# Performance work log

Hardware: AMD Instinct MI355X
Metric: run time of the kernel (lower is better)

The kernel has to match this reference:

```python
import jax, jax.numpy as jnp
import numpy as np

KERNEL_SIZE = 7      # odd, per assert in __init__
MAX_VAL = 1e4        # kornia morphology default max_val


def setup_inputs() -> dict:
    key = jax.random.key(0)
    kx, ka, kb, kc = jax.random.split(key, 4)
    x = jax.random.normal(kx, (8, 64, 256, 256), dtype=jnp.float32)
    k1 = jax.random.uniform(ka, (1,), dtype=jnp.float32)
    k2 = jax.random.uniform(kb, (1,), dtype=jnp.float32)
    k3 = jax.random.uniform(kc, (1,), dtype=jnp.float32)
    return {"x": x, "k1": k1, "k2": k2, "k3": k3}


def _structuring_element(k1, k2, k3):
    k = KERNEL_SIZE
    # torch.arange(-k//2 + 1, k//2 + 1) with floor-div == -(k//2)..k//2 for odd k
    c = jnp.arange(-(k // 2), k // 2 + 1, dtype=jnp.float32)
    xg, yg = jnp.meshgrid(c, c, indexing='xy')
    se = k1[0] * xg ** 2 + 2.0 * k2[0] * xg * yg + k3[0] * yg ** 2
    se = se / se.max()
    return -se  # (k, k)


def reference(x, k1, k2, k3):
    k = KERNEL_SIZE
    se = _structuring_element(k1, k2, k3)
    # flat kernel of ones with center zeroed -> center tap masked to -max_val
    mask = np.ones((k, k), dtype=bool)
    mask[k // 2, k // 2] = False
    neighborhood = jnp.where(jnp.asarray(mask), se, -MAX_VAL)
    nb = neighborhood[::-1, ::-1]  # kornia dilation flips the neighborhood

    pad = k // 2
    # geodesic border for dilation: pad with -max_val
    xp = jnp.pad(x, ((0, 0), (0, 0), (pad, pad), (pad, pad)),
                 constant_values=-MAX_VAL)
    H, W = x.shape[-2], x.shape[-1]
    # fused running max over the k*k taps; avoids materializing the unfold
    out = jnp.full_like(x, -jnp.inf)
    for i in range(k):
        for j in range(k):
            out = jnp.maximum(out, xp[..., i:i + H, j:j + W] + nb[i, j])
    return out
```

## Files before the change

kernel.cpp:

```cpp
#include <hip/hip_runtime.h>


#define MAXV 10000.0f

constexpr int H = 256;
constexpr int W = 256;
constexpr int TILE_ROWS = 16;
constexpr int LDS_ROWS = TILE_ROWS + 6;
constexpr int LDS_STRIDE = 264;
constexpr int ROW_TILES = H / TILE_ROWS;
constexpr int R = 4;

__device__ __forceinline__ float rfl(float x) {
  return __int_as_float(__builtin_amdgcn_readfirstlane(__float_as_int(x)));
}

__global__ __launch_bounds__(256, 6) void morpho_kernel(
    const float* __restrict__ x,
    const float* __restrict__ k1p,
    const float* __restrict__ k2p,
    const float* __restrict__ k3p,
    float* __restrict__ out) {
  __shared__ __align__(16) float tile[LDS_ROWS * LDS_STRIDE];

  const int tid = threadIdx.x;
  const int p = blockIdx.x >> 4;
  const int ty0 = (blockIdx.x & 15) * TILE_ROWS;

  const float* __restrict__ xp = x + (size_t)p * (H * W);
  float* __restrict__ op = out + (size_t)p * (H * W);

  if (tid < LDS_ROWS * 8) {
    const int h = tid & 7;
    const int col = (h < 4) ? h : (256 + h);
    const int r = tid >> 3;
    tile[r * LDS_STRIDE + col] = -MAXV;
  }

  for (int i = tid; i < LDS_ROWS * 64; i += 256) {
    const int r = i >> 6;
    const int c4 = i & 63;
    const int gy = ty0 - 3 + r;
    float4 v;
    if ((unsigned)gy < (unsigned)H) {
      v = *reinterpret_cast<const float4*>(&xp[gy * W + c4 * 4]);
    } else {
      v.x = v.y = v.z = v.w = -MAXV;
    }
    *reinterpret_cast<float4*>(&tile[r * LDS_STRIDE + 4 + c4 * 4]) = v;
  }

  const float k1v = k1p[0], k2v = k2p[0], k3v = k3p[0];
  float se[49];
#pragma unroll
  for (int i = 0; i < 49; ++i) {
    const float xg = (float)(i % 7 - 3);
    const float yg = (float)(i / 7 - 3);
    se[i] = k1v * (xg * xg) + 2.0f * k2v * (xg * yg) + k3v * (yg * yg);
  }
  float m = se[0];
#pragma unroll
  for (int i = 1; i < 49; ++i) m = fmaxf(m, se[i]);
  const float inv = 1.0f / m;
  float w[49];
#pragma unroll
  for (int i = 0; i < 49; ++i) w[i] = rfl((i == 24) ? -MAXV : (0.0f - se[i] * inv));

  __syncthreads();

  const int tx = tid & 63;
  const int g = tid >> 6;
  const int r0 = g * R;

  float acc[R][4];
#pragma unroll
  for (int t = 0; t < R; ++t)
#pragma unroll
    for (int c = 0; c < 4; ++c) acc[t][c] = -INFINITY;

#pragma unroll
  for (int iy = 0; iy < R + 6; ++iy) {
    const float* rp = &tile[(r0 + iy) * LDS_STRIDE + tx * 4];
    float buf[12];
#pragma unroll
    for (int q = 0; q < 3; ++q) {
      const float4 v = *reinterpret_cast<const float4*>(rp + 4 * q);
      buf[4 * q + 0] = v.x;
      buf[4 * q + 1] = v.y;
      buf[4 * q + 2] = v.z;
      buf[4 * q + 3] = v.w;
    }
#pragma unroll
    for (int t = 0; t < R; ++t) {
      const int dyr = iy - t;
      if (dyr < 0 || dyr > 6) continue;
#pragma unroll
      for (int c = 0; c < 4; ++c) {
        const float s0 = buf[c + 1] + w[dyr * 7 + 0];
        const float s1 = buf[c + 2] + w[dyr * 7 + 1];
        const float s2 = buf[c + 3] + w[dyr * 7 + 2];
        const float s3 = buf[c + 4] + w[dyr * 7 + 3];
        const float s4 = buf[c + 5] + w[dyr * 7 + 4];
        const float s5 = buf[c + 6] + w[dyr * 7 + 5];
        const float s6 = buf[c + 7] + w[dyr * 7 + 6];
        const float m0 = fmaxf(fmaxf(s0, s1), s2);
        const float m1 = fmaxf(fmaxf(s3, s4), s5);
        const float m01 = fmaxf(m0, m1);
        acc[t][c] = fmaxf(acc[t][c], fmaxf(m01, s6));
      }
    }
  }

#pragma unroll
  for (int t = 0; t < R; ++t) {
    const int gy = ty0 + r0 + t;
    float4 v;
    v.x = acc[t][0];
    v.y = acc[t][1];
    v.z = acc[t][2];
    v.w = acc[t][3];
    *reinterpret_cast<float4*>(&op[gy * W + tx * 4]) = v;
  }
}

extern "C" void kernel_launch(void* const* d_in, const int* in_sizes, int n_in,
                              void* d_out, int out_size, void* d_ws, size_t ws_size,
                              hipStream_t stream) {
  const float* x = (const float*)d_in[0];
  const float* k1 = (const float*)d_in[1];
  const float* k2 = (const float*)d_in[2];
  const float* k3 = (const float*)d_in[3];
  float* outp = (float*)d_out;

  const int planes = 8 * 64;
  const int blocks = planes * ROW_TILES;
  morpho_kernel<<<dim3(blocks), dim3(256), 0, stream>>>(x, k1, k2, k3, outp);
}
```

Baseline: 287.1 us.

## Load tile via direct global-to-LDS loads, lane-parallel weights, nontemporal stores

```diff
diff --git a/kernel.cpp b/kernel.cpp
--- a/kernel.cpp
+++ b/kernel.cpp
@@ -11,8 +11,12 @@
 constexpr int ROW_TILES = H / TILE_ROWS;
 constexpr int R = 4;
 
-__device__ __forceinline__ float rfl(float x) {
-  return __int_as_float(__builtin_amdgcn_readfirstlane(__float_as_int(x)));
+typedef float vfloat4 __attribute__((ext_vector_type(4)));
+
+__device__ __forceinline__ void load_lds16(const float* g, float* l) {
+  __builtin_amdgcn_global_load_lds(
+      (const __attribute__((address_space(1))) void*)g,
+      (__attribute__((address_space(3))) void*)l, 16, 0, 0);
 }
 
 __global__ __launch_bounds__(256, 6) void morpho_kernel(
@@ -24,53 +28,52 @@
   __shared__ __align__(16) float tile[LDS_ROWS * LDS_STRIDE];
 
   const int tid = threadIdx.x;
+  const int lane = tid & 63;
+  const int wid = tid >> 6;
   const int p = blockIdx.x >> 4;
   const int ty0 = (blockIdx.x & 15) * TILE_ROWS;
 
   const float* __restrict__ xp = x + (size_t)p * (H * W);
   float* __restrict__ op = out + (size_t)p * (H * W);
 
+  for (int r = wid; r < LDS_ROWS; r += 4) {
+    const int gy = ty0 - 3 + r;
+    float* ldst = &tile[r * LDS_STRIDE + 4];
+    if ((unsigned)gy < (unsigned)H) {
+      load_lds16(&xp[gy * W + lane * 4], ldst);
+    } else {
+      vfloat4 mv = {-MAXV, -MAXV, -MAXV, -MAXV};
+      *reinterpret_cast<vfloat4*>(ldst + lane * 4) = mv;
+    }
+  }
+
   if (tid < LDS_ROWS * 8) {
     const int h = tid & 7;
     const int col = (h < 4) ? h : (256 + h);
-    const int r = tid >> 3;
-    tile[r * LDS_STRIDE + col] = -MAXV;
-  }
-
-  for (int i = tid; i < LDS_ROWS * 64; i += 256) {
-    const int r = i >> 6;
-    const int c4 = i & 63;
-    const int gy = ty0 - 3 + r;
-    float4 v;
-    if ((unsigned)gy < (unsigned)H) {
-      v = *reinterpret_cast<const float4*>(&xp[gy * W + c4 * 4]);
-    } else {
-      v.x = v.y = v.z = v.w = -MAXV;
-    }
-    *reinterpret_cast<float4*>(&tile[r * LDS_STRIDE + 4 + c4 * 4]) = v;
+    tile[(tid >> 3) * LDS_STRIDE + col] = -MAXV;
   }
 
   const float k1v = k1p[0], k2v = k2p[0], k3v = k3p[0];
-  float se[49];
+  const int a = lane >> 3, b = lane & 7;
+  const float xg = (float)(((b < 6) ? b : 6) - 3);
+  const float yg = (float)(((a < 6) ? a : 6) - 3);
+  const float sev = k1v * (xg * xg) + 2.0f * k2v * (xg * yg) + k3v * (yg * yg);
+  float mx = sev;
+#pragma unroll
+  for (int off = 32; off; off >>= 1) mx = fmaxf(mx, __shfl_xor(mx, off, 64));
+  const float wv = 0.0f - sev * (1.0f / mx);
+
+  float w[49];
 #pragma unroll
   for (int i = 0; i < 49; ++i) {
-    const float xg = (float)(i % 7 - 3);
-    const float yg = (float)(i / 7 - 3);
-    se[i] = k1v * (xg * xg) + 2.0f * k2v * (xg * yg) + k3v * (yg * yg);
+    const int src = (i / 7) * 8 + (i % 7);
+    w[i] = __int_as_float(__builtin_amdgcn_readlane(__float_as_int(wv), src));
   }
-  float m = se[0];
-#pragma unroll
-  for (int i = 1; i < 49; ++i) m = fmaxf(m, se[i]);
-  const float inv = 1.0f / m;
-  float w[49];
-#pragma unroll
-  for (int i = 0; i < 49; ++i) w[i] = rfl((i == 24) ? -MAXV : (0.0f - se[i] * inv));
+  w[24] = -MAXV;
 
   __syncthreads();
 
-  const int tx = tid & 63;
-  const int g = tid >> 6;
-  const int r0 = g * R;
+  const int r0 = wid * R;
 
   float acc[R][4];
 #pragma unroll
@@ -80,11 +83,11 @@
 
 #pragma unroll
   for (int iy = 0; iy < R + 6; ++iy) {
-    const float* rp = &tile[(r0 + iy) * LDS_STRIDE + tx * 4];
+    const float* rp = &tile[(r0 + iy) * LDS_STRIDE + lane * 4];
     float buf[12];
 #pragma unroll
     for (int q = 0; q < 3; ++q) {
-      const float4 v = *reinterpret_cast<const float4*>(rp + 4 * q);
+      const vfloat4 v = *reinterpret_cast<const vfloat4*>(rp + 4 * q);
       buf[4 * q + 0] = v.x;
       buf[4 * q + 1] = v.y;
       buf[4 * q + 2] = v.z;
@@ -114,12 +117,12 @@
 #pragma unroll
   for (int t = 0; t < R; ++t) {
     const int gy = ty0 + r0 + t;
-    float4 v;
+    vfloat4 v;
     v.x = acc[t][0];
     v.y = acc[t][1];
     v.z = acc[t][2];
     v.w = acc[t][3];
-    *reinterpret_cast<float4*>(&op[gy * W + tx * 4]) = v;
+    __builtin_nontemporal_store(v, reinterpret_cast<vfloat4*>(&op[gy * W + lane * 4]));
   }
 }
 
```

After: 486.4 us. +69.4%, slower.
